# Kernel tuning notes

Hardware: AMD Instinct MI355X
Metric: run time of the kernel (lower is better)

The kernel has to match this reference:

```python
import jax, jax.numpy as jnp
import numpy as np

N_NODES = 100000
N_EDGES = 1600000
N_GRAPHS = 512
IN_DIM = 3
HIDDEN = 128


def setup_inputs() -> dict:
    key = jax.random.key(0)
    ks = jax.random.split(key, 8)
    x = jax.random.normal(ks[0], (N_NODES, IN_DIM), dtype=jnp.float32)
    edge_index = jax.random.randint(ks[1], (2, N_EDGES), 0, N_NODES, dtype=jnp.int64)
    batch = jnp.sort(jax.random.randint(ks[2], (N_NODES,), 0, N_GRAPHS, dtype=jnp.int64))
    W1 = jax.random.normal(ks[3], (IN_DIM, HIDDEN), dtype=jnp.float32) / np.sqrt(IN_DIM)
    b1 = jnp.zeros((HIDDEN,), dtype=jnp.float32)
    W2 = jax.random.normal(ks[4], (HIDDEN, HIDDEN), dtype=jnp.float32) / np.sqrt(HIDDEN)
    b2 = jnp.zeros((HIDDEN,), dtype=jnp.float32)
    Wc = jax.random.normal(ks[5], (HIDDEN, 1), dtype=jnp.float32) / np.sqrt(HIDDEN)
    bc = jnp.zeros((1,), dtype=jnp.float32)
    return {"x": x, "edge_index": edge_index, "batch": batch,
            "W1": W1, "b1": b1, "W2": W2, "b2": b2, "Wc": Wc, "bc": bc}


def _gcn_conv(x, W, b, src, dst, n_nodes):
    # PyG GCNConv: h = X W; add self-loops; symmetric norm D^-1/2 (A+I) D^-1/2; scatter-add; + bias
    h = x @ W  # [N, H]
    deg = jax.ops.segment_sum(jnp.ones_like(dst, dtype=h.dtype), dst, num_segments=n_nodes) + 1.0  # +1 self-loop
    dinv = jax.lax.rsqrt(deg)  # [N]
    norm = dinv[src] * dinv[dst]  # [E]
    msg = h[src] * norm[:, None]  # [E, H] gather + scale
    agg = jax.ops.segment_sum(msg, dst, num_segments=n_nodes)  # scatter-add
    agg = agg + h * (dinv * dinv)[:, None]  # self-loop contribution
    return agg + b


def reference(x, edge_index, batch, W1, b1, W2, b2, Wc, bc):
    src, dst = edge_index[0], edge_index[1]
    n = x.shape[0]
    h = jax.nn.relu(_gcn_conv(x, W1, b1, src, dst, n))
    h = jax.nn.relu(_gcn_conv(h, W2, b2, src, dst, n))
    # global mean pool over graphs
    sums = jax.ops.segment_sum(h, batch, num_segments=N_GRAPHS)  # [G, H]
    cnt = jax.ops.segment_sum(jnp.ones((n,), dtype=h.dtype), batch, num_segments=N_GRAPHS)
    pooled = sums / jnp.maximum(cnt, 1.0)[:, None]
    logits = pooled @ Wc + bc  # [G, 1]
    return jax.nn.sigmoid(logits).squeeze(-1)  # [G]
```

## Files before the change

kernel.cpp:

```cpp
#include <hip/hip_runtime.h>
#include <hip/hip_bf16.h>
#include <math.h>

#define H 128
#define NTPB 256
#define NBKT 256
#define BSH 9
#define BMSK 511
#define EPB 8192
#define POOL_CHUNK 2048

typedef __attribute__((ext_vector_type(8))) short short8;
typedef __attribute__((ext_vector_type(4))) float floatx4;
typedef __attribute__((ext_vector_type(2))) float f2v;

__device__ __forceinline__ void atomAddF(float* p, float v) {
    __hip_atomic_fetch_add(p, v, __ATOMIC_RELAXED, __HIP_MEMORY_SCOPE_AGENT);
}

__device__ __forceinline__ short f2bf(float v) {
    __hip_bfloat16 b = __float2bfloat16(v);
    return __builtin_bit_cast(short, b);
}

__device__ __forceinline__ f2v splat2(float v) { return (f2v){v, v}; }

__global__ void hist_kernel(const int* __restrict__ ei, int E, int* __restrict__ ghist) {
    __shared__ int lh[NBKT];
    int t = threadIdx.x;
    lh[t] = 0;
    __syncthreads();
    int base = blockIdx.x * EPB;
#pragma unroll
    for (int k = 0; k < EPB / NTPB; k++) {
        int e = base + k * NTPB + t;
        if (e < E) atomicAdd(&lh[((unsigned)ei[E + e]) >> BSH], 1);
    }
    __syncthreads();
    if (lh[t]) atomicAdd(&ghist[t], lh[t]);
}

__global__ void scan_buckets(const int* __restrict__ ghist, int* __restrict__ gbase,
                             int* __restrict__ gcursor) {
    __shared__ int sd[NBKT];
    int t = threadIdx.x;
    int v = ghist[t];
    sd[t] = v; __syncthreads();
    for (int s = 1; s < NBKT; s <<= 1) {
        int u = (t >= s) ? sd[t - s] : 0;
        __syncthreads();
        sd[t] += u;
        __syncthreads();
    }
    int ex = sd[t] - v;
    gbase[t] = ex;
    gcursor[t] = ex;
    if (t == NBKT - 1) gbase[NBKT] = sd[t];
}

__global__ void partition_kernel(const int* __restrict__ ei, int E,
                                 int* __restrict__ gcursor, unsigned* __restrict__ ebuf) {
    __shared__ int lcur[NBKT];
    __shared__ int lbase[NBKT];
    int t = threadIdx.x;
    lcur[t] = 0;
    __syncthreads();
    int base = blockIdx.x * EPB;
    unsigned short rk[EPB / NTPB];
#pragma unroll
    for (int k = 0; k < EPB / NTPB; k++) {
        int e = base + k * NTPB + t;
        rk[k] = 0;
        if (e < E) rk[k] = (unsigned short)atomicAdd(&lcur[((unsigned)ei[E + e]) >> BSH], 1);
    }
    __syncthreads();
    lbase[t] = atomicAdd(&gcursor[t], lcur[t]);
    __syncthreads();
#pragma unroll
    for (int k = 0; k < EPB / NTPB; k++) {
        int e = base + k * NTPB + t;
        if (e < E) {
            unsigned d = (unsigned)ei[E + e];
            unsigned s = (unsigned)ei[e];
            ebuf[lbase[d >> BSH] + rk[k]] = ((d & BMSK) << 17) | s;
        }
    }
}

__global__ void bucket_sort(const unsigned* __restrict__ ebuf, const int* __restrict__ gbase,
                            const float* __restrict__ x,
                            int* __restrict__ rowptr, unsigned* __restrict__ csr,
                            float4* __restrict__ xs4, int N) {
    __shared__ int ldeg[512];
    __shared__ int loff[512];
    __shared__ int sd[NTPB];
    int t = threadIdx.x, b = blockIdx.x;
    int node0 = b << BSH;
    int beg = gbase[b], end = gbase[b + 1];
    ldeg[t] = 0; ldeg[t + 256] = 0;
    __syncthreads();
    for (int i = beg + t; i < end; i += NTPB)
        atomicAdd(&ldeg[ebuf[i] >> 17], 1);
    __syncthreads();
    int d0 = ldeg[2 * t], d1 = ldeg[2 * t + 1];
    int ps = d0 + d1;
    sd[t] = ps; __syncthreads();
    for (int s = 1; s < NTPB; s <<= 1) {
        int u = (t >= s) ? sd[t - s] : 0;
        __syncthreads();
        sd[t] += u;
        __syncthreads();
    }
    int ex = sd[t] - ps;
    loff[2 * t] = ex;
    loff[2 * t + 1] = ex + d0;
    __syncthreads();
    for (int i = t; i < 512; i += NTPB) {
        int node = node0 + i;
        if (node < N) {
            rowptr[node] = beg + loff[i];
            float dv = rsqrtf((float)(ldeg[i] + 1));
            xs4[node] = make_float4(x[3 * node] * dv, x[3 * node + 1] * dv,
                                    x[3 * node + 2] * dv, dv);
        } else if (node == N) {
            rowptr[N] = beg + loff[i];
        }
    }
    __syncthreads();
    for (int i = beg + t; i < end; i += NTPB) {
        unsigned u = ebuf[i];
        int pos = beg + atomicAdd(&loff[u >> 17], 1);
        csr[pos] = u & 0x1FFFFu;
    }
}

__global__ void bpack_kernel(const float* __restrict__ W2, __hip_bfloat16* __restrict__ Bp) {
    int idx = blockIdx.x * blockDim.x + threadIdx.x;
    if (idx >= 2048) return;
    int frag = idx >> 6, lane = idx & 63;
    int nt = frag >> 2, c = frag & 3, quad = lane >> 4, m16 = lane & 15;
#pragma unroll
    for (int jj = 0; jj < 8; jj++) {
        int k = c * 32 + quad * 8 + jj;
        Bp[idx * 8 + jj] = __float2bfloat16(W2[k * H + nt * 16 + m16]);
    }
}

__global__ void l1_gather(const float4* __restrict__ xs4,
                          const int* __restrict__ rowptr, const unsigned* __restrict__ csr,
                          float4* __restrict__ aggx4, int N) {
    int n = blockIdx.x * blockDim.x + threadIdx.x;
    if (n >= N) return;
    float4 xn = xs4[n];
    float a0 = xn.x, a1 = xn.y, a2 = xn.z;
    int beg = rowptr[n], end = rowptr[n + 1];
    int i = beg;
    for (; i + 4 <= end; i += 4) {
        float4 q0 = xs4[csr[i]];
        float4 q1 = xs4[csr[i + 1]];
        float4 q2 = xs4[csr[i + 2]];
        float4 q3 = xs4[csr[i + 3]];
        a0 += q0.x + q1.x + q2.x + q3.x;
        a1 += q0.y + q1.y + q2.y + q3.y;
        a2 += q0.z + q1.z + q2.z + q3.z;
    }
    for (; i < end; ++i) {
        float4 q = xs4[csr[i]];
        a0 += q.x; a1 += q.y; a2 += q.z;
    }
    float dv = xn.w;
    aggx4[n] = make_float4(a0 * dv, a1 * dv, a2 * dv, dv);
}

__device__ __forceinline__ void edge_acc(const float4 p, const f2v wa, const f2v wb,
                                         const f2v wc, const f2v bb, f2v& acc) {
    f2v z = __builtin_elementwise_fma(splat2(p.x), wa, bb);
    z = __builtin_elementwise_fma(splat2(p.y), wb, z);
    z = __builtin_elementwise_fma(splat2(p.z), wc, z);
    z = __builtin_elementwise_max(z, (f2v){0.f, 0.f});
    acc = __builtin_elementwise_fma(splat2(p.w), z, acc);
}

__global__ void l2_gather(
        const float4* __restrict__ aggx4,
        const int* __restrict__ rowptr, const unsigned* __restrict__ csr,
        const float* __restrict__ W1, const float* __restrict__ b1,
        __hip_bfloat16* __restrict__ agg1, int N) {
    int t = threadIdx.x;
    int lane = t & 63;
    int node = __builtin_amdgcn_readfirstlane(blockIdx.x * 4 + (t >> 6));
    if (node >= N) return;
    int k0 = 2 * lane;
    f2v wa = *(const f2v*)&W1[k0];
    f2v wb = *(const f2v*)&W1[H + k0];
    f2v wc = *(const f2v*)&W1[2 * H + k0];
    f2v bb = *(const f2v*)&b1[k0];
    f2v acc = (f2v){0.f, 0.f};
    int beg = rowptr[node], end = rowptr[node + 1];
    int i = beg;
    for (; i + 4 <= end; i += 4) {
        unsigned s0 = csr[i], s1 = csr[i + 1], s2 = csr[i + 2], s3 = csr[i + 3];
        float4 p0 = aggx4[s0];
        float4 p1 = aggx4[s1];
        float4 p2 = aggx4[s2];
        float4 p3 = aggx4[s3];
        edge_acc(p0, wa, wb, wc, bb, acc);
        edge_acc(p1, wa, wb, wc, bb, acc);
        edge_acc(p2, wa, wb, wc, bb, acc);
        edge_acc(p3, wa, wb, wc, bb, acc);
    }
    for (; i < end; ++i) {
        float4 p = aggx4[csr[i]];
        edge_acc(p, wa, wb, wc, bb, acc);
    }
    float4 ps = aggx4[node];
    edge_acc(ps, wa, wb, wc, bb, acc);
    float dv = ps.w;
    f2v r = acc * splat2(dv);
    unsigned packed = ((unsigned)(unsigned short)f2bf(r.x)) |
                      ((unsigned)(unsigned short)f2bf(r.y) << 16);
    ((unsigned*)agg1)[(size_t)node * (H / 2) + lane] = packed;
}

__global__ __launch_bounds__(NTPB, 4) void gemm_nodedot(
        const __hip_bfloat16* __restrict__ agg1, const __hip_bfloat16* __restrict__ Bp,
        const float* __restrict__ b2, const float* __restrict__ Wc,
        float* __restrict__ nodedot, int N) {
    __shared__ float sb2[H];
    __shared__ float swc[H];
    int t = threadIdx.x;
    if (t < H) { sb2[t] = b2[t]; swc[t] = Wc[t]; }
    __syncthreads();
    int wave = t >> 6, lane = t & 63;
    int quad = lane >> 4, m16 = lane & 15;
    int tile = blockIdx.x * 4 + wave;
    int rowbase = tile * 16;
    if (rowbase >= N) return;
    int m = rowbase + m16;
    const short8* as8 = (const short8*)agg1;
    short8 af[4];
    if (m < N) {
#pragma unroll
        for (int c = 0; c < 4; c++) af[c] = as8[(size_t)m * 16 + c * 4 + quad];
    } else {
#pragma unroll
        for (int c = 0; c < 4; c++) af[c] = (short8){0, 0, 0, 0, 0, 0, 0, 0};
    }
    const short8* bp = (const short8*)Bp;
    floatx4 acc[8];
#pragma unroll
    for (int nt = 0; nt < 8; nt++) acc[nt] = (floatx4){0.f, 0.f, 0.f, 0.f};
#pragma unroll
    for (int nt = 0; nt < 8; nt++) {
#pragma unroll
        for (int c = 0; c < 4; c++) {
            short8 bf = bp[(nt * 4 + c) * 64 + lane];
            acc[nt] = __builtin_amdgcn_mfma_f32_16x16x32_bf16(af[c], bf, acc[nt], 0, 0, 0);
        }
    }
    float dot0 = 0.f, dot1 = 0.f, dot2 = 0.f, dot3 = 0.f;
#pragma unroll
    for (int nt = 0; nt < 8; nt++) {
        int col = nt * 16 + m16;
        float bcol = sb2[col], wcol = swc[col];
        dot0 += fmaxf(acc[nt][0] + bcol, 0.f) * wcol;
        dot1 += fmaxf(acc[nt][1] + bcol, 0.f) * wcol;
        dot2 += fmaxf(acc[nt][2] + bcol, 0.f) * wcol;
        dot3 += fmaxf(acc[nt][3] + bcol, 0.f) * wcol;
    }
#pragma unroll
    for (int s = 1; s < 16; s <<= 1) {
        dot0 += __shfl_xor(dot0, s);
        dot1 += __shfl_xor(dot1, s);
        dot2 += __shfl_xor(dot2, s);
        dot3 += __shfl_xor(dot3, s);
    }
    if (m16 < 4) {
        int row = rowbase + quad * 4 + m16;
        if (row < N) {
            float d = (m16 == 0) ? dot0 : (m16 == 1) ? dot1 : (m16 == 2) ? dot2 : dot3;
            nodedot[row] = d;
        }
    }
}

__global__ void pool_kernel(const float* __restrict__ nodedot, const int* __restrict__ batch,
                            float* __restrict__ gsum, int* __restrict__ gcnt, int N, int G) {
    extern __shared__ char sm[];
    float* ls = (float*)sm;
    int*   lc = (int*)(sm + (size_t)G * sizeof(float));
    int t = threadIdx.x;
    for (int g = t; g < G; g += blockDim.x) { ls[g] = 0.f; lc[g] = 0; }
    __syncthreads();
    int base = blockIdx.x * POOL_CHUNK;
    int endn = min(base + POOL_CHUNK, N);
    for (int n = base + t; n < endn; n += blockDim.x) {
        int g = batch[n];
        atomicAdd(&ls[g], nodedot[n]);
        atomicAdd(&lc[g], 1);
    }
    __syncthreads();
    for (int g = t; g < G; g += blockDim.x) {
        if (lc[g] != 0) {
            atomAddF(&gsum[g], ls[g]);
            atomicAdd(&gcnt[g], lc[g]);
        }
    }
}

__global__ void out_kernel(const float* __restrict__ gsum, const int* __restrict__ gcnt,
                           const float* __restrict__ bc, float* __restrict__ out, int G) {
    int g = blockIdx.x * blockDim.x + threadIdx.x;
    if (g >= G) return;
    float c = fmaxf((float)gcnt[g], 1.f);
    float logit = gsum[g] / c + bc[0];
    out[g] = 1.f / (1.f + expf(-logit));
}

extern "C" void kernel_launch(void* const* d_in, const int* in_sizes, int n_in,
                              void* d_out, int out_size, void* d_ws, size_t ws_size,
                              hipStream_t stream) {
    const float* x     = (const float*)d_in[0];
    const int*   ei    = (const int*)d_in[1];
    const int*   batch = (const int*)d_in[2];
    const float* W1    = (const float*)d_in[3];
    const float* b1    = (const float*)d_in[4];
    const float* W2    = (const float*)d_in[5];
    const float* b2    = (const float*)d_in[6];
    const float* Wc    = (const float*)d_in[7];
    const float* bc    = (const float*)d_in[8];
    float* out = (float*)d_out;

    int N = in_sizes[2];
    int E = in_sizes[1] / 2;
    int G = out_size;

    char* ws = (char*)d_ws;
    size_t off = 0;
    auto alloc = [&](size_t bytes) {
        void* p = ws + off;
        off += (bytes + 255) & ~(size_t)255;
        return p;
    };
    __hip_bfloat16* agg1 = (__hip_bfloat16*)alloc((size_t)N * H * sizeof(__hip_bfloat16));
    float4* xs4   = (float4*)alloc((size_t)N * sizeof(float4));
    float4* aggx4 = (float4*)alloc((size_t)N * sizeof(float4));
    float* nodedot= (float*)alloc((size_t)N * sizeof(float));
    float* gsum   = (float*)alloc((size_t)G * sizeof(float));
    int*   gcnt   = (int*)  alloc((size_t)G * sizeof(int));
    int*   ghist  = (int*)  alloc((size_t)NBKT * sizeof(int));
    char*  zero_end = ws + off;
    int*   gbase  = (int*)  alloc((size_t)(NBKT + 1) * sizeof(int));
    int*   gcursor= (int*)  alloc((size_t)NBKT * sizeof(int));
    int*   rowptr = (int*)  alloc((size_t)(N + 1) * sizeof(int));
    unsigned* csr = (unsigned*)alloc((size_t)E * sizeof(unsigned));
    unsigned* ebuf= (unsigned*)alloc((size_t)E * sizeof(unsigned));
    __hip_bfloat16* Bp = (__hip_bfloat16*)alloc((size_t)H * H * sizeof(__hip_bfloat16));

    (void)hipMemsetAsync(gsum, 0, (size_t)(zero_end - (char*)gsum), stream);

    int EB = (E + EPB - 1) / EPB;
    hist_kernel<<<EB, NTPB, 0, stream>>>(ei, E, ghist);
    scan_buckets<<<1, NBKT, 0, stream>>>(ghist, gbase, gcursor);
    partition_kernel<<<EB, NTPB, 0, stream>>>(ei, E, gcursor, ebuf);
    {
        int nbs = (N >> BSH) + 1;
        bucket_sort<<<nbs, NTPB, 0, stream>>>(ebuf, gbase, x, rowptr, csr, xs4, N);
    }

    bpack_kernel<<<8, NTPB, 0, stream>>>(W2, Bp);

    l1_gather<<<(N + NTPB - 1) / NTPB, NTPB, 0, stream>>>(xs4, rowptr, csr, aggx4, N);

    l2_gather<<<(N + 3) / 4, NTPB, 0, stream>>>(aggx4, rowptr, csr, W1, b1, agg1, N);

    {
        int ntiles = (N + 15) / 16;
        gemm_nodedot<<<(ntiles + 3) / 4, NTPB, 0, stream>>>(agg1, Bp, b2, Wc, nodedot, N);
    }

    {
        int pblocks = (N + POOL_CHUNK - 1) / POOL_CHUNK;
        size_t smem = (size_t)G * (sizeof(float) + sizeof(int));
        pool_kernel<<<pblocks, NTPB, smem, stream>>>(nodedot, batch, gsum, gcnt, N, G);
    }

    out_kernel<<<(G + NTPB - 1) / NTPB, NTPB, 0, stream>>>(gsum, gcnt, bc, out, G);
}
```

Measured before the change: 230.7 us.

## Process 16 nodes per wave in l2_gather with cooperative lane-parallel edge loads

l2_gather now assigns 16 consecutive destination nodes to each wave instead of one. The wave loads CSR neighbour indices and their aggx4 float4 values cooperatively, one edge per lane and 64 at a time, with one 64-edge block prefetched ahead. Each edge's values are then broadcast to all lanes with readlane. This replaces redundant uniform per-lane loads with coalesced vector loads and amortises setup across nodes. In exchange the loop becomes serial per edge with four readlanes each, and the csr and aggx4 buffers are padded and indices masked so the over-reads at the end stay in bounds.

```diff
diff --git a/kernel.cpp b/kernel.cpp
--- a/kernel.cpp
+++ b/kernel.cpp
@@ -9,6 +9,8 @@
 #define BMSK 511
 #define EPB 8192
 #define POOL_CHUNK 2048
+#define SRC_MASK 0x1FFFFu
+#define NPW 16
 
 typedef __attribute__((ext_vector_type(8))) short short8;
 typedef __attribute__((ext_vector_type(4))) float floatx4;
@@ -24,6 +26,10 @@
 }
 
 __device__ __forceinline__ f2v splat2(float v) { return (f2v){v, v}; }
+
+__device__ __forceinline__ float rdlane(float v, int sl) {
+    return __int_as_float(__builtin_amdgcn_readlane(__float_as_int(v), sl));
+}
 
 __global__ void hist_kernel(const int* __restrict__ ei, int E, int* __restrict__ ghist) {
     __shared__ int lh[NBKT];
@@ -172,13 +178,14 @@
     aggx4[n] = make_float4(a0 * dv, a1 * dv, a2 * dv, dv);
 }
 
-__device__ __forceinline__ void edge_acc(const float4 p, const f2v wa, const f2v wb,
-                                         const f2v wc, const f2v bb, f2v& acc) {
-    f2v z = __builtin_elementwise_fma(splat2(p.x), wa, bb);
-    z = __builtin_elementwise_fma(splat2(p.y), wb, z);
-    z = __builtin_elementwise_fma(splat2(p.z), wc, z);
+__device__ __forceinline__ void edge_accs(float px, float py, float pz, float pw,
+                                          const f2v wa, const f2v wb, const f2v wc,
+                                          const f2v bb, f2v& acc) {
+    f2v z = __builtin_elementwise_fma(splat2(px), wa, bb);
+    z = __builtin_elementwise_fma(splat2(py), wb, z);
+    z = __builtin_elementwise_fma(splat2(pz), wc, z);
     z = __builtin_elementwise_max(z, (f2v){0.f, 0.f});
-    acc = __builtin_elementwise_fma(splat2(p.w), z, acc);
+    acc = __builtin_elementwise_fma(splat2(pw), z, acc);
 }
 
 __global__ void l2_gather(
@@ -188,38 +195,46 @@
         __hip_bfloat16* __restrict__ agg1, int N) {
     int t = threadIdx.x;
     int lane = t & 63;
-    int node = __builtin_amdgcn_readfirstlane(blockIdx.x * 4 + (t >> 6));
-    if (node >= N) return;
+    int wave = blockIdx.x * (NTPB / 64) + (t >> 6);
+    int n0 = wave * NPW;
+    if (n0 >= N) return;
+    int nEnd = min(n0 + NPW, N);
     int k0 = 2 * lane;
     f2v wa = *(const f2v*)&W1[k0];
     f2v wb = *(const f2v*)&W1[H + k0];
     f2v wc = *(const f2v*)&W1[2 * H + k0];
     f2v bb = *(const f2v*)&b1[k0];
-    f2v acc = (f2v){0.f, 0.f};
-    int beg = rowptr[node], end = rowptr[node + 1];
+    float4 own = aggx4[min(n0 + (lane & (NPW - 1)), N - 1)];
+    int rpl = rowptr[min(n0 + min(lane, NPW), N)];
+    int beg = __builtin_amdgcn_readlane(rpl, 0);
+    int qb = beg;
+    float4 qA = aggx4[csr[qb + lane] & SRC_MASK];
+    float4 qB = aggx4[csr[qb + 64 + lane] & SRC_MASK];
+    unsigned cN = csr[qb + 128 + lane];
     int i = beg;
-    for (; i + 4 <= end; i += 4) {
-        unsigned s0 = csr[i], s1 = csr[i + 1], s2 = csr[i + 2], s3 = csr[i + 3];
-        float4 p0 = aggx4[s0];
-        float4 p1 = aggx4[s1];
-        float4 p2 = aggx4[s2];
-        float4 p3 = aggx4[s3];
-        edge_acc(p0, wa, wb, wc, bb, acc);
-        edge_acc(p1, wa, wb, wc, bb, acc);
-        edge_acc(p2, wa, wb, wc, bb, acc);
-        edge_acc(p3, wa, wb, wc, bb, acc);
-    }
-    for (; i < end; ++i) {
-        float4 p = aggx4[csr[i]];
-        edge_acc(p, wa, wb, wc, bb, acc);
-    }
-    float4 ps = aggx4[node];
-    edge_acc(ps, wa, wb, wc, bb, acc);
-    float dv = ps.w;
-    f2v r = acc * splat2(dv);
-    unsigned packed = ((unsigned)(unsigned short)f2bf(r.x)) |
-                      ((unsigned)(unsigned short)f2bf(r.y) << 16);
-    ((unsigned*)agg1)[(size_t)node * (H / 2) + lane] = packed;
+    for (int n = n0; n < nEnd; ++n) {
+        int re = __builtin_amdgcn_readlane(rpl, n - n0 + 1);
+        f2v acc = (f2v){0.f, 0.f};
+        for (; i < re; ++i) {
+            if (i == qb + 64) {
+                qA = qB;
+                qb += 64;
+                qB = aggx4[cN & SRC_MASK];
+                cN = csr[qb + 128 + lane];
+            }
+            int sl = i - qb;
+            edge_accs(rdlane(qA.x, sl), rdlane(qA.y, sl),
+                      rdlane(qA.z, sl), rdlane(qA.w, sl), wa, wb, wc, bb, acc);
+        }
+        int sn = n - n0;
+        float ox = rdlane(own.x, sn), oy = rdlane(own.y, sn);
+        float oz = rdlane(own.z, sn), ow = rdlane(own.w, sn);
+        edge_accs(ox, oy, oz, ow, wa, wb, wc, bb, acc);
+        f2v r = acc * splat2(ow);
+        unsigned packed = ((unsigned)(unsigned short)f2bf(r.x)) |
+                          ((unsigned)(unsigned short)f2bf(r.y) << 16);
+        ((unsigned*)agg1)[(size_t)n * (H / 2) + lane] = packed;
+    }
 }
 
 __global__ __launch_bounds__(NTPB, 4) void gemm_nodedot(
@@ -344,7 +359,7 @@
     };
     __hip_bfloat16* agg1 = (__hip_bfloat16*)alloc((size_t)N * H * sizeof(__hip_bfloat16));
     float4* xs4   = (float4*)alloc((size_t)N * sizeof(float4));
-    float4* aggx4 = (float4*)alloc((size_t)N * sizeof(float4));
+    float4* aggx4 = (float4*)alloc((size_t)(SRC_MASK + 1) * sizeof(float4));
     float* nodedot= (float*)alloc((size_t)N * sizeof(float));
     float* gsum   = (float*)alloc((size_t)G * sizeof(float));
     int*   gcnt   = (int*)  alloc((size_t)G * sizeof(int));
@@ -353,7 +368,7 @@
     int*   gbase  = (int*)  alloc((size_t)(NBKT + 1) * sizeof(int));
     int*   gcursor= (int*)  alloc((size_t)NBKT * sizeof(int));
     int*   rowptr = (int*)  alloc((size_t)(N + 1) * sizeof(int));
-    unsigned* csr = (unsigned*)alloc((size_t)E * sizeof(unsigned));
+    unsigned* csr = (unsigned*)alloc((size_t)(E + 256) * sizeof(unsigned));
     unsigned* ebuf= (unsigned*)alloc((size_t)E * sizeof(unsigned));
     __hip_bfloat16* Bp = (__hip_bfloat16*)alloc((size_t)H * H * sizeof(__hip_bfloat16));
 
@@ -372,7 +387,11 @@
 
     l1_gather<<<(N + NTPB - 1) / NTPB, NTPB, 0, stream>>>(xs4, rowptr, csr, aggx4, N);
 
-    l2_gather<<<(N + 3) / 4, NTPB, 0, stream>>>(aggx4, rowptr, csr, W1, b1, agg1, N);
+    {
+        int waves = (N + NPW - 1) / NPW;
+        int blocks = (waves + (NTPB / 64) - 1) / (NTPB / 64);
+        l2_gather<<<blocks, NTPB, 0, stream>>>(aggx4, rowptr, csr, W1, b1, agg1, N);
+    }
 
     {
         int ntiles = (N + 15) / 16;
```

Result: slower. 262.0 us (+13.6%).
